# Performance work log

Hardware: AMD Instinct MI355X
Metric: run time of the kernel (lower is better)

## Reference

```python
import jax, jax.numpy as jnp
import numpy as np

N = 50000      # nodes
E = 800000     # directed edges (avg degree 16)
IN, HID, OUT = 256, 128, 16


def setup_inputs() -> dict:
    key = jax.random.key(0)
    ks = jax.random.split(key, 8)
    x = jax.random.normal(ks[0], (N, IN), dtype=jnp.float32)
    edge_index = jax.random.randint(ks[1], (2, E), 0, N)
    W1 = jax.random.normal(ks[2], (IN, HID), dtype=jnp.float32) * (1.0 / np.sqrt(IN))
    b1 = jnp.zeros((HID,), jnp.float32)
    W2 = jax.random.normal(ks[3], (HID, HID), dtype=jnp.float32) * (1.0 / np.sqrt(HID))
    b2 = jnp.zeros((HID,), jnp.float32)
    Wc = jax.random.normal(ks[4], (HID, OUT), dtype=jnp.float32) * (1.0 / np.sqrt(HID))
    bc = jnp.zeros((OUT,), jnp.float32)
    return {"x": x, "W1": W1, "b1": b1, "W2": W2, "b2": b2,
            "Wc": Wc, "bc": bc, "edge_index": edge_index, "conv_time": 30}


def _gcn_norm(edge_index, n, dtype):
    # add self-loops, compute symmetric GCN normalization D^{-1/2}(A+I)D^{-1/2}
    loops = jnp.arange(n)
    src = jnp.concatenate([edge_index[0], loops])
    dst = jnp.concatenate([edge_index[1], loops])
    deg = jax.ops.segment_sum(jnp.ones_like(dst, dtype=dtype), dst, num_segments=n)
    dinv = jnp.where(deg > 0, jax.lax.rsqrt(deg), jnp.zeros_like(deg))
    norm = dinv[src] * dinv[dst]          # [E+N] edge weights
    return src, dst, norm


def _propagate(h, src, dst, norm, n, hops):
    # hops is a static Python int (conv_time)
    for _ in range(hops):
        h = jax.ops.segment_sum(h[src] * norm[:, None], dst, num_segments=n)
    return h


def reference(x, W1, b1, W2, b2, Wc, bc, edge_index, conv_time):
    n = x.shape[0]
    src, dst, norm = _gcn_norm(edge_index, n, x.dtype)
    # conv1: linear only (conv_time = 0)
    h = jax.nn.relu(x @ W1 + b1)
    # dropout is identity in eval mode
    # conv2: linear + conv_time hops of normalized propagation
    h = _propagate(h @ W2 + b2, src, dst, norm, n, int(conv_time))
    h = jax.nn.relu(h)
    # cls: linear + 1 hop
    h = _propagate(h @ Wc + bc, src, dst, norm, n, 1)
    return h
```

## Files before the change

kernel.cpp:

```cpp
#include <hip/hip_runtime.h>
#include <hip/hip_fp16.h>

#define NNODES 50000
#define NEDGES 800000
#define IN_F   256
#define HID_F  128
#define OUT_F  16
#define HOPS   30

typedef unsigned int u32;

union U32H2 { u32 u; __half2 h; };

__device__ inline float2 upk(u32 v) {
    U32H2 t; t.u = v;
    return __half22float2(t.h);
}
__device__ inline u32 pk2(float a, float b) {
    U32H2 t; t.h = __floats2half2_rn(a, b);
    return t.u;
}


__global__ void k_init_deg(int* __restrict__ deg, int n) {
    int i = blockIdx.x * blockDim.x + threadIdx.x;
    if (i < n) deg[i] = 1;
}

__global__ void k_count(const int* __restrict__ dst, int* __restrict__ deg, int e) {
    int i = blockIdx.x * blockDim.x + threadIdx.x;
    if (i < e) atomicAdd(&deg[dst[i]], 1);
}

__global__ void k_dinv(const int* __restrict__ deg, float* __restrict__ dinv, int n) {
    int i = blockIdx.x * blockDim.x + threadIdx.x;
    if (i < n) dinv[i] = rsqrtf((float)deg[i]);
}

__global__ void k_scan1(const int* __restrict__ deg, int* __restrict__ bsums, int n) {
    __shared__ int sh[256];
    int tid = threadIdx.x;
    int i = blockIdx.x * 256 + tid;
    sh[tid] = (i < n) ? deg[i] : 0;
    __syncthreads();
    for (int ofs = 128; ofs > 0; ofs >>= 1) {
        if (tid < ofs) sh[tid] += sh[tid + ofs];
        __syncthreads();
    }
    if (tid == 0) bsums[blockIdx.x] = sh[0];
}

__global__ void k_scan2(int* __restrict__ bsums, int nb, int* __restrict__ rp, int n) {
    if (threadIdx.x == 0 && blockIdx.x == 0) {
        int run = 0;
        for (int b = 0; b < nb; ++b) { int t = bsums[b]; bsums[b] = run; run += t; }
        rp[n] = run;
    }
}

__global__ void k_scan3(const int* __restrict__ deg, const int* __restrict__ bsums,
                        int* __restrict__ rp, int* __restrict__ cursor, int n) {
    __shared__ int sh[256];
    int tid = threadIdx.x;
    int i = blockIdx.x * 256 + tid;
    int v = (i < n) ? deg[i] : 0;
    sh[tid] = v;
    __syncthreads();
    for (int ofs = 1; ofs < 256; ofs <<= 1) {
        int t = 0;
        if (tid >= ofs) t = sh[tid - ofs];
        __syncthreads();
        sh[tid] += t;
        __syncthreads();
    }
    if (i < n) {
        int excl = sh[tid] - v + bsums[blockIdx.x];
        rp[i] = excl;
        cursor[i] = excl;
    }
}

__global__ void k_scatter(const int* __restrict__ src, const int* __restrict__ dst,
                          const float* __restrict__ dinv, int* __restrict__ cursor,
                          int2* __restrict__ ew, int e, int n) {
    int t = blockIdx.x * blockDim.x + threadIdx.x;
    if (t < e) {
        int s = src[t], d = dst[t];
        int pos = atomicAdd(&cursor[d], 1);
        ew[pos] = make_int2(s, __float_as_int(dinv[s] * dinv[d]));
    } else if (t < e + n) {
        int i = t - e;
        int pos = atomicAdd(&cursor[i], 1);
        float di = dinv[i];
        ew[pos] = make_int2(i, __float_as_int(di * di));
    }
}

__global__ void k_sortwave(const int* __restrict__ rp, int2* __restrict__ ew, int n) {
    int node = blockIdx.x * 4 + (threadIdx.x >> 6);
    int lane = threadIdx.x & 63;
    if (node >= n) return;
    int beg = rp[node], end = rp[node + 1];
    int deg = end - beg;
    if (deg > 64) return;
    int2 my = make_int2(0x7fffffff, 0);
    if (lane < deg) my = ew[beg + lane];
    int rank = 0;
#pragma unroll 8
    for (int k = 0; k < 64; ++k) {
        int sk = __shfl(my.x, k);
        rank += (sk < my.x) || (sk == my.x && k < lane);
    }
    if (lane < deg) ew[beg + rank] = my;
}


template<int K, bool RELU, bool HALF_OUT>
__global__ void k_gemm32(const float* __restrict__ A, const float* __restrict__ W,
                         const float* __restrict__ b, void* __restrict__ C, int M) {
    __shared__ float sa[32][K];
    int tid  = threadIdx.x;
    int row0 = blockIdx.x * 32;
    constexpr int KV = K / 4;

    const float4* A4 = reinterpret_cast<const float4*>(A);
    for (int idx = tid; idx < 32 * KV; idx += 256) {
        int r  = idx / KV;
        int c4 = idx % KV;
        int gr = row0 + r;
        float4 v = (gr < M) ? A4[(size_t)gr * KV + c4]
                            : make_float4(0.f, 0.f, 0.f, 0.f);
        *reinterpret_cast<float4*>(&sa[r][c4 * 4]) = v;
    }
    __syncthreads();

    int tc = tid & 31;
    int tr = tid >> 5;
    float4 acc[4];
#pragma unroll
    for (int j = 0; j < 4; ++j) acc[j] = make_float4(0.f, 0.f, 0.f, 0.f);

    const float4* W4 = reinterpret_cast<const float4*>(W);
    float4 wv[4];
#pragma unroll
    for (int kk = 0; kk < 4; ++kk) wv[kk] = W4[(size_t)kk * 32 + tc];

    for (int k4 = 0; k4 < KV; ++k4) {
        float4 wn[4];
        if (k4 + 1 < KV) {
#pragma unroll
            for (int kk = 0; kk < 4; ++kk)
                wn[kk] = W4[(size_t)((k4 + 1) * 4 + kk) * 32 + tc];
        } else {
#pragma unroll
            for (int kk = 0; kk < 4; ++kk) wn[kk] = wv[kk];
        }
        float4 a[4];
#pragma unroll
        for (int j = 0; j < 4; ++j)
            a[j] = *reinterpret_cast<const float4*>(&sa[tr * 4 + j][k4 * 4]);
        const float* af = reinterpret_cast<const float*>(a);
#pragma unroll
        for (int kk = 0; kk < 4; ++kk) {
#pragma unroll
            for (int j = 0; j < 4; ++j) {
                float av = af[j * 4 + kk];
                acc[j].x += av * wv[kk].x; acc[j].y += av * wv[kk].y;
                acc[j].z += av * wv[kk].z; acc[j].w += av * wv[kk].w;
            }
        }
#pragma unroll
        for (int kk = 0; kk < 4; ++kk) wv[kk] = wn[kk];
    }

    float4 bb = reinterpret_cast<const float4*>(b)[tc];
#pragma unroll
    for (int j = 0; j < 4; ++j) {
        int r = row0 + tr * 4 + j;
        if (r < M) {
            float4 v;
            v.x = acc[j].x + bb.x; v.y = acc[j].y + bb.y;
            v.z = acc[j].z + bb.z; v.w = acc[j].w + bb.w;
            if (RELU) {
                v.x = fmaxf(v.x, 0.f); v.y = fmaxf(v.y, 0.f);
                v.z = fmaxf(v.z, 0.f); v.w = fmaxf(v.w, 0.f);
            }
            if (HALF_OUT) {
                u32 lo = pk2(v.x, v.y), hi = pk2(v.z, v.w);
                reinterpret_cast<uint2*>(C)[(size_t)r * 32 + tc] = make_uint2(lo, hi);
            } else {
                reinterpret_cast<float4*>(C)[(size_t)r * 32 + tc] = v;
            }
        }
    }
}


template<bool RELU>
__global__ void k_proph(const u32* __restrict__ Hin, u32* __restrict__ Hout,
                        const int* __restrict__ rp, const int2* __restrict__ ew,
                        int n) {
    int grp  = threadIdx.x >> 4;
    int lane = threadIdx.x & 15;
    int node = blockIdx.x * 16 + grp;
    if (node >= n) return;
    int beg = rp[node], end = rp[node + 1];
    const uint4* H4 = reinterpret_cast<const uint4*>(Hin);

    float acc[8];
#pragma unroll
    for (int i = 0; i < 8; ++i) acc[i] = 0.f;

    auto body = [&](int e) {
        int2 p   = ew[e];
        float ww = __int_as_float(p.y);
        uint4 v  = H4[(size_t)p.x * 16 + lane];
        const u32* vv = reinterpret_cast<const u32*>(&v);
#pragma unroll
        for (int q = 0; q < 4; ++q) {
            float2 f = upk(vv[q]);
            acc[q * 2 + 0] += ww * f.x;
            acc[q * 2 + 1] += ww * f.y;
        }
    };

    int e = beg;
    for (; e + 1 < end; e += 2) { body(e); body(e + 1); }
    if (e < end) body(e);

    if (RELU) {
#pragma unroll
        for (int i = 0; i < 8; ++i) acc[i] = fmaxf(acc[i], 0.f);
    }
    uint4 o;
    u32* ov = reinterpret_cast<u32*>(&o);
#pragma unroll
    for (int q = 0; q < 4; ++q) ov[q] = pk2(acc[q * 2], acc[q * 2 + 1]);
    reinterpret_cast<uint4*>(Hout)[(size_t)node * 16 + lane] = o;
}


__global__ void k_cls_h(const u32* __restrict__ Ah, const float* __restrict__ Wc,
                        const float* __restrict__ bc, float* __restrict__ G, int M) {
    __shared__ float sa[64][132];
    __shared__ float4 sw4[512];
    int tid  = threadIdx.x;
    int row0 = blockIdx.x * 64;

    for (int idx = tid; idx < 512; idx += 256)
        sw4[idx] = reinterpret_cast<const float4*>(Wc)[idx];

    const uint4* A4 = reinterpret_cast<const uint4*>(Ah);
    for (int idx = tid; idx < 64 * 16; idx += 256) {
        int r = idx >> 4, c = idx & 15;
        int gr = row0 + r;
        uint4 v = (gr < M) ? A4[(size_t)gr * 16 + c]
                           : make_uint4(0u, 0u, 0u, 0u);
        float* dst = &sa[r][c * 8];
        const u32* vv = reinterpret_cast<const u32*>(&v);
#pragma unroll
        for (int q = 0; q < 4; ++q) {
            float2 f = upk(vv[q]);
            dst[q * 2 + 0] = f.x;
            dst[q * 2 + 1] = f.y;
        }
    }
    __syncthreads();

    int tc = tid & 3;
    int tr = tid >> 2;
    float4 acc = make_float4(0.f, 0.f, 0.f, 0.f);
    for (int k4 = 0; k4 < 32; ++k4) {
        float4 a = *reinterpret_cast<const float4*>(&sa[tr][k4 * 4]);
        const float* af = reinterpret_cast<const float*>(&a);
#pragma unroll
        for (int kk = 0; kk < 4; ++kk) {
            float4 wv = sw4[(k4 * 4 + kk) * 4 + tc];
            float av = af[kk];
            acc.x += av * wv.x; acc.y += av * wv.y;
            acc.z += av * wv.z; acc.w += av * wv.w;
        }
    }
    int r = row0 + tr;
    if (r < M) {
        float4 bb = reinterpret_cast<const float4*>(bc)[tc];
        acc.x += bb.x; acc.y += bb.y; acc.z += bb.z; acc.w += bb.w;
        reinterpret_cast<float4*>(G)[(size_t)r * 4 + tc] = acc;
    }
}


__global__ void k_prop16(const float* __restrict__ Gin, float* __restrict__ Out,
                         const int* __restrict__ rp, const int2* __restrict__ ew,
                         int n) {
    int g    = blockIdx.x * 64 + (threadIdx.x >> 2);
    int lane = threadIdx.x & 3;
    if (g >= n) return;
    int beg = rp[g], end = rp[g + 1];
    const float4* G4 = reinterpret_cast<const float4*>(Gin);
    float ax = 0.f, ay = 0.f, az = 0.f, aw = 0.f;
    for (int e = beg; e < end; ++e) {
        int2 p   = ew[e];
        float ww = __int_as_float(p.y);
        float4 hv = G4[(size_t)p.x * 4 + lane];
        ax += ww * hv.x; ay += ww * hv.y; az += ww * hv.z; aw += ww * hv.w;
    }
    reinterpret_cast<float4*>(Out)[(size_t)g * 4 + lane] = make_float4(ax, ay, az, aw);
}


extern "C" void kernel_launch(void* const* d_in, const int* in_sizes, int n_in,
                              void* d_out, int out_size, void* d_ws, size_t ws_size,
                              hipStream_t stream) {
    const float* x  = (const float*)d_in[0];
    const float* W1 = (const float*)d_in[1];
    const float* b1 = (const float*)d_in[2];
    const float* W2 = (const float*)d_in[3];
    const float* b2 = (const float*)d_in[4];
    const float* Wc = (const float*)d_in[5];
    const float* bc = (const float*)d_in[6];
    const int*   ei = (const int*)d_in[7];
    const int* srcp = ei;
    const int* dstp = ei + NEDGES;
    float* out = (float*)d_out;

    char* p = (char*)d_ws;
    auto alloc = [&](size_t bytes) -> char* {
        char* r = p;
        p += (bytes + 255) & ~(size_t)255;
        return r;
    };
    int*   deg    = (int*)  alloc(NNODES * 4);
    float* dinv   = (float*)alloc(NNODES * 4);
    int*   rp     = (int*)  alloc((NNODES + 1) * 4);
    int*   cursor = (int*)  alloc(NNODES * 4);
    int*   bsums  = (int*)  alloc(256 * 4);
    int2*  ew     = (int2*) alloc((size_t)(NEDGES + NNODES) * 8);
    float* H0     = (float*)alloc((size_t)NNODES * HID_F * 4);
    u32*   Hh0    = (u32*)  alloc((size_t)NNODES * HID_F * 2);
    u32*   Hh1    = (u32*)  alloc((size_t)NNODES * HID_F * 2);
    float* G      = (float*)alloc((size_t)NNODES * OUT_F * 4);

    const int T = 256;
    auto nb = [](int n, int t) { return (n + t - 1) / t; };

    k_init_deg<<<nb(NNODES, T), T, 0, stream>>>(deg, NNODES);
    k_count<<<nb(NEDGES, T), T, 0, stream>>>(dstp, deg, NEDGES);
    k_dinv<<<nb(NNODES, T), T, 0, stream>>>(deg, dinv, NNODES);
    int NB = nb(NNODES, 256);
    k_scan1<<<NB, 256, 0, stream>>>(deg, bsums, NNODES);
    k_scan2<<<1, 1, 0, stream>>>(bsums, NB, rp, NNODES);
    k_scan3<<<NB, 256, 0, stream>>>(deg, bsums, rp, cursor, NNODES);
    k_scatter<<<nb(NEDGES + NNODES, T), T, 0, stream>>>(srcp, dstp, dinv, cursor,
                                                        ew, NEDGES, NNODES);
    k_sortwave<<<nb(NNODES, 4), 256, 0, stream>>>(rp, ew, NNODES);

    int GB = nb(NNODES, 32);
    k_gemm32<IN_F,  true,  false><<<GB, 256, 0, stream>>>(x,  W1, b1, H0,  NNODES);
    k_gemm32<HID_F, false, true ><<<GB, 256, 0, stream>>>(H0, W2, b2, Hh0, NNODES);

    u32* cur = Hh0;
    u32* nxt = Hh1;
    int PB = nb(NNODES, 16);
    for (int i = 0; i < HOPS; ++i) {
        if (i == HOPS - 1)
            k_proph<true ><<<PB, 256, 0, stream>>>(cur, nxt, rp, ew, NNODES);
        else
            k_proph<false><<<PB, 256, 0, stream>>>(cur, nxt, rp, ew, NNODES);
        u32* t = cur; cur = nxt; nxt = t;
    }

    k_cls_h<<<nb(NNODES, 64), 256, 0, stream>>>(cur, Wc, bc, G, NNODES);
    k_prop16<<<nb(NNODES, 64), 256, 0, stream>>>(G, out, rp, ew, NNODES);
}
```

Measured before the change: 1.144 ms.

## Replace FP32 SIMT GEMMs with FP16 MFMA GEMMs for both linear layers

Casts x and the transposed weights to fp16 in separate kernels, then computes both dense layers with MFMA 16x16x32 f16 instructions instead of scalar FP32 FMAs. The intermediate H0 is now fp16, which halves its traffic. The GEMMs are a small part of the runtime next to the 30 propagation hops, and the extra cast pass over x adds memory traffic. It also lowers the precision of the first layer. The padded buffers xh and H0h, sized MPAD, are read past NNODES without being initialised.

```diff
diff --git a/kernel.cpp b/kernel.cpp
--- a/kernel.cpp
+++ b/kernel.cpp
@@ -7,8 +7,12 @@
 #define HID_F  128
 #define OUT_F  16
 #define HOPS   30
+#define MPAD   50048
 
 typedef unsigned int u32;
+typedef _Float16 f16;
+typedef f16 f16x8 __attribute__((ext_vector_type(8)));
+typedef float f32x4 __attribute__((ext_vector_type(4)));
 
 union U32H2 { u32 u; __half2 h; };
 
@@ -115,81 +119,64 @@
 }
 
 
-template<int K, bool RELU, bool HALF_OUT>
-__global__ void k_gemm32(const float* __restrict__ A, const float* __restrict__ W,
-                         const float* __restrict__ b, void* __restrict__ C, int M) {
-    __shared__ float sa[32][K];
-    int tid  = threadIdx.x;
-    int row0 = blockIdx.x * 32;
-    constexpr int KV = K / 4;
-
-    const float4* A4 = reinterpret_cast<const float4*>(A);
-    for (int idx = tid; idx < 32 * KV; idx += 256) {
-        int r  = idx / KV;
-        int c4 = idx % KV;
-        int gr = row0 + r;
-        float4 v = (gr < M) ? A4[(size_t)gr * KV + c4]
-                            : make_float4(0.f, 0.f, 0.f, 0.f);
-        *reinterpret_cast<float4*>(&sa[r][c4 * 4]) = v;
-    }
-    __syncthreads();
-
-    int tc = tid & 31;
-    int tr = tid >> 5;
-    float4 acc[4];
-#pragma unroll
-    for (int j = 0; j < 4; ++j) acc[j] = make_float4(0.f, 0.f, 0.f, 0.f);
-
-    const float4* W4 = reinterpret_cast<const float4*>(W);
-    float4 wv[4];
-#pragma unroll
-    for (int kk = 0; kk < 4; ++kk) wv[kk] = W4[(size_t)kk * 32 + tc];
-
-    for (int k4 = 0; k4 < KV; ++k4) {
-        float4 wn[4];
-        if (k4 + 1 < KV) {
-#pragma unroll
-            for (int kk = 0; kk < 4; ++kk)
-                wn[kk] = W4[(size_t)((k4 + 1) * 4 + kk) * 32 + tc];
-        } else {
-#pragma unroll
-            for (int kk = 0; kk < 4; ++kk) wn[kk] = wv[kk];
-        }
-        float4 a[4];
-#pragma unroll
-        for (int j = 0; j < 4; ++j)
-            a[j] = *reinterpret_cast<const float4*>(&sa[tr * 4 + j][k4 * 4]);
-        const float* af = reinterpret_cast<const float*>(a);
-#pragma unroll
-        for (int kk = 0; kk < 4; ++kk) {
-#pragma unroll
-            for (int j = 0; j < 4; ++j) {
-                float av = af[j * 4 + kk];
-                acc[j].x += av * wv[kk].x; acc[j].y += av * wv[kk].y;
-                acc[j].z += av * wv[kk].z; acc[j].w += av * wv[kk].w;
-            }
-        }
-#pragma unroll
-        for (int kk = 0; kk < 4; ++kk) wv[kk] = wn[kk];
-    }
-
-    float4 bb = reinterpret_cast<const float4*>(b)[tc];
-#pragma unroll
-    for (int j = 0; j < 4; ++j) {
-        int r = row0 + tr * 4 + j;
-        if (r < M) {
-            float4 v;
-            v.x = acc[j].x + bb.x; v.y = acc[j].y + bb.y;
-            v.z = acc[j].z + bb.z; v.w = acc[j].w + bb.w;
-            if (RELU) {
-                v.x = fmaxf(v.x, 0.f); v.y = fmaxf(v.y, 0.f);
-                v.z = fmaxf(v.z, 0.f); v.w = fmaxf(v.w, 0.f);
-            }
-            if (HALF_OUT) {
-                u32 lo = pk2(v.x, v.y), hi = pk2(v.z, v.w);
-                reinterpret_cast<uint2*>(C)[(size_t)r * 32 + tc] = make_uint2(lo, hi);
-            } else {
-                reinterpret_cast<float4*>(C)[(size_t)r * 32 + tc] = v;
+__global__ void k_cast_x(const float* __restrict__ in, f16* __restrict__ out, int n) {
+    int i = blockIdx.x * blockDim.x + threadIdx.x;
+    int stride = gridDim.x * blockDim.x;
+    for (; i < n / 4; i += stride) {
+        float4 v = reinterpret_cast<const float4*>(in)[i];
+        f16 o[4] = {(f16)v.x, (f16)v.y, (f16)v.z, (f16)v.w};
+        *reinterpret_cast<uint2*>(&reinterpret_cast<f16*>(out)[i * 4]) =
+            *reinterpret_cast<uint2*>(o);
+    }
+}
+
+template<int K, int NC>
+__global__ void k_cast_wt(const float* __restrict__ W, f16* __restrict__ Wt) {
+    int i = blockIdx.x * blockDim.x + threadIdx.x;
+    if (i < K * NC) {
+        int k = i / NC, c = i % NC;
+        Wt[(size_t)c * K + k] = (f16)W[i];
+    }
+}
+
+
+template<int K, bool RELU>
+__global__ __launch_bounds__(256)
+void k_gemm_mfma(const f16* __restrict__ A, const f16* __restrict__ Wt,
+                 const float* __restrict__ b, f16* __restrict__ C, int M) {
+    int wid  = threadIdx.x >> 6;
+    int lane = threadIdx.x & 63;
+    int rowW = blockIdx.x * 64 + wid * 16;
+    int rl   = lane & 15;
+    int kc   = (lane >> 4) * 8;
+
+    f32x4 acc[8];
+#pragma unroll
+    for (int n = 0; n < 8; ++n) acc[n] = (f32x4)0.f;
+
+    const f16* Arow = A + (size_t)(rowW + rl) * K;
+#pragma unroll
+    for (int k0 = 0; k0 < K; k0 += 32) {
+        f16x8 aF = *reinterpret_cast<const f16x8*>(Arow + k0 + kc);
+#pragma unroll
+        for (int n = 0; n < 8; ++n) {
+            f16x8 bF = *reinterpret_cast<const f16x8*>(
+                Wt + (size_t)(n * 16 + rl) * K + k0 + kc);
+            acc[n] = __builtin_amdgcn_mfma_f32_16x16x32_f16(aF, bF, acc[n], 0, 0, 0);
+        }
+    }
+
+#pragma unroll
+    for (int n = 0; n < 8; ++n) {
+        int col = n * 16 + rl;
+        float bias = b[col];
+#pragma unroll
+        for (int j = 0; j < 4; ++j) {
+            int row = rowW + 4 * (lane >> 4) + j;
+            if (row < M) {
+                float s = acc[n][j] + bias;
+                if (RELU) s = fmaxf(s, 0.f);
+                C[(size_t)row * 128 + col] = (f16)s;
             }
         }
     }
@@ -336,7 +323,10 @@
     int*   cursor = (int*)  alloc(NNODES * 4);
     int*   bsums  = (int*)  alloc(256 * 4);
     int2*  ew     = (int2*) alloc((size_t)(NEDGES + NNODES) * 8);
-    float* H0     = (float*)alloc((size_t)NNODES * HID_F * 4);
+    f16*   xh     = (f16*)  alloc((size_t)MPAD * IN_F * 2);
+    f16*   W1t    = (f16*)  alloc((size_t)HID_F * IN_F * 2);
+    f16*   W2t    = (f16*)  alloc((size_t)HID_F * HID_F * 2);
+    f16*   H0h    = (f16*)  alloc((size_t)MPAD * HID_F * 2);
     u32*   Hh0    = (u32*)  alloc((size_t)NNODES * HID_F * 2);
     u32*   Hh1    = (u32*)  alloc((size_t)NNODES * HID_F * 2);
     float* G      = (float*)alloc((size_t)NNODES * OUT_F * 4);
@@ -355,9 +345,13 @@
                                                         ew, NEDGES, NNODES);
     k_sortwave<<<nb(NNODES, 4), 256, 0, stream>>>(rp, ew, NNODES);
 
-    int GB = nb(NNODES, 32);
-    k_gemm32<IN_F,  true,  false><<<GB, 256, 0, stream>>>(x,  W1, b1, H0,  NNODES);
-    k_gemm32<HID_F, false, true ><<<GB, 256, 0, stream>>>(H0, W2, b2, Hh0, NNODES);
+    k_cast_x<<<1024, 256, 0, stream>>>(x, xh, NNODES * IN_F);
+    k_cast_wt<IN_F,  HID_F><<<nb(IN_F * HID_F, T), T, 0, stream>>>(W1, W1t);
+    k_cast_wt<HID_F, HID_F><<<nb(HID_F * HID_F, T), T, 0, stream>>>(W2, W2t);
+
+    int GB = MPAD / 64;
+    k_gemm_mfma<IN_F,  true ><<<GB, 256, 0, stream>>>(xh,  W1t, b1, H0h, NNODES);
+    k_gemm_mfma<HID_F, false><<<GB, 256, 0, stream>>>(H0h, W2t, b2, (f16*)Hh0, NNODES);
 
     u32* cur = Hh0;
     u32* nxt = Hh1;
```

Measured after the change: 1.122 ms. 2.0% less time.
